# Performance work log

Measured on AMD Instinct MI355X. Metric: run time of the kernel, lower is better.

The kernel has to match this reference:

```python
import jax, jax.numpy as jnp
import numpy as np

TEMPERATURE = 0.5  # init temperature; attn_drop=0.0 so dropout is identity


def setup_inputs() -> dict:
    key = jax.random.key(0)
    k1, k2, k3 = jax.random.split(key, 3)
    B, H, N, D = 4, 8, 2048, 64
    q = jax.random.normal(k1, (B, H, N, D), dtype=jnp.float32)
    k = jax.random.normal(k2, (B, H, N, D), dtype=jnp.float32)
    v = jax.random.normal(k3, (B, H, N, D), dtype=jnp.float32)
    scale = jnp.asarray(D ** -0.5, dtype=jnp.float32)
    return {"q": q, "k": k, "v": v, "scale": scale}


def reference(q, k, v, scale):
    # logits: [B,H,N,N]
    logits = jnp.einsum("bhqd,bhkd->bhqk", q, k) * scale
    # first softmax acts as a soft mask over keys
    soft_mask = jax.nn.softmax(logits / TEMPERATURE, axis=-1)
    # second softmax over masked logits (elementwise product, NOT matmul)
    attn = jax.nn.softmax(logits * soft_mask, axis=-1)
    # dropout with p=0.0 is identity
    out = jnp.einsum("bhqk,bhkd->bhqd", attn, v)
    return out
```

## Files before the change

### kernel.cpp

```cpp
#include <hip/hip_runtime.h>


typedef _Float16 f16;
typedef f16 f16x8 __attribute__((ext_vector_type(8)));
typedef f16 f16x4 __attribute__((ext_vector_type(4)));
typedef float f32x4 __attribute__((ext_vector_type(4)));

#define MFMA32(a, b, c) __builtin_amdgcn_mfma_f32_16x16x32_f16((a), (b), (c), 0, 0, 0)
#define MFMA16(a, b, c) __builtin_amdgcn_mfma_f32_16x16x16f16((a), (b), (c), 0, 0, 0)
#define EXP2(x) __builtin_amdgcn_exp2f(x)

#define N_CTX 2048
#define DH 64
#define KT 64
#define NKT_G 16
#define ROWS 128
#define QS 72
#define KSB (KT * QS)
#define SMEM_BYTES (4 * 2 * KSB * 2 + 2048)

#define C2 2.885390081777927f

__device__ inline unsigned pk(float a, float b) {
    typedef __fp16 fp16x2_t __attribute__((ext_vector_type(2)));
    union { fp16x2_t v; unsigned u; } x;
    x.v = __builtin_amdgcn_cvt_pkrtz(a, b);
    return x.u;
}

__global__ __launch_bounds__(256)
void stk_prep(const float* __restrict__ kg, const float* __restrict__ vg,
              f16* __restrict__ wsK, f16* __restrict__ wsV) {
    const int bid = blockIdx.x, tid = threadIdx.x;
    if (bid < 2048) {
        int g = bid * 256 + tid;
        int bh = g >> 14, key = (g >> 3) & 2047, c = g & 7;
        const float* src = kg + (((size_t)bh * 2048 + key) << 6) + c * 8;
        float4 a = *(const float4*)src;
        float4 b = *(const float4*)(src + 4);
        uint4 o;
        o.x = pk(a.x, a.y); o.y = pk(a.z, a.w);
        o.z = pk(b.x, b.y); o.w = pk(b.z, b.w);
        *(uint4*)&wsK[(((size_t)bh * 2048 + key) << 6) + c * 8] = o;
    } else {
        __shared__ f16 lds[DH * QS];
        const int bid2 = bid - 2048;
        const int bh = bid2 >> 5, t = bid2 & 31;
        const int p = tid >> 3, dseg = tid & 7, d0 = dseg * 8;
        const int c0 = ((p >> 1) & 3) * 16 + ((p >> 3) & 3) * 4 + (p & 1) * 2;
        const float* base = vg + (((size_t)(bh * 2048 + t * 64 + 2 * p)) << 6) + d0;
        float4 a0 = *(const float4*)(base);
        float4 a1 = *(const float4*)(base + 4);
        float4 b0 = *(const float4*)(base + 64);
        float4 b1 = *(const float4*)(base + 68);
        #pragma unroll
        for (int j = 0; j < 4; ++j) {
            *(unsigned*)&lds[(d0 + j) * QS + c0] =
                pk(((const float*)&a0)[j], ((const float*)&b0)[j]);
            *(unsigned*)&lds[(d0 + 4 + j) * QS + c0] =
                pk(((const float*)&a1)[j], ((const float*)&b1)[j]);
        }
        __syncthreads();
        const int d = tid >> 2, cs = tid & 3;
        f16x8 r0 = *(const f16x8*)&lds[d * QS + cs * 16];
        f16x8 r1 = *(const f16x8*)&lds[d * QS + cs * 16 + 8];
        f16* dst = wsV + ((((size_t)bh * 32 + t) << 6) + d) * 64 + cs * 16;
        *(f16x8*)(dst) = r0;
        *(f16x8*)(dst + 8) = r1;
    }
}

__global__ __launch_bounds__(1024, 8)
void stk_attn_mfma(const float* __restrict__ qg, const f16* __restrict__ wsK,
                   const f16* __restrict__ wsV, const float* __restrict__ sg,
                   float* __restrict__ og) {
    extern __shared__ f16 smem[];

    const int tid  = threadIdx.x;
    const int wv   = tid >> 6;
    const int grp  = wv >> 3;
    const int wv7  = wv & 7;
    const int lane = tid & 63;
    const int l15  = lane & 15;
    const int q4   = lane >> 4;
    const int tg   = (wv7 << 6) | lane;
    const int bh   = blockIdx.x & 31;
    const int q0   = (blockIdx.x >> 5) * ROWS;
    const float scale2 = sg[0] * C2;

    const float* qb = qg + (size_t)bh * N_CTX * DH;
    float*       ob = og + (size_t)bh * N_CTX * DH;
    const f16* wsKh = wsK + ((size_t)bh << 17);
    const f16* wsVh = wsV + ((size_t)bh << 17);
    const int T0 = grp * NKT_G;

    f16x8 aq[2];
    {
        const float* qrow = qb + (size_t)(q0 + wv7 * 16 + l15) * DH;
        #pragma unroll
        for (int kc = 0; kc < 2; ++kc) {
            float4 a0 = *(const float4*)&qrow[kc * 32 + q4 * 8];
            float4 a1 = *(const float4*)&qrow[kc * 32 + q4 * 8 + 4];
            union { f16x8 h; unsigned u[4]; } A;
            A.u[0] = pk(a0.x * scale2, a0.y * scale2);
            A.u[1] = pk(a0.z * scale2, a0.w * scale2);
            A.u[2] = pk(a1.x * scale2, a1.y * scale2);
            A.u[3] = pk(a1.z * scale2, a1.w * scale2);
            aq[kc] = A.h;
        }
    }

    f16* const ksBase = smem + grp * (2 * KSB);
    f16* const vtBase = smem + 2 * (2 * KSB) + grp * (2 * KSB);
    float* const sred = (float*)(smem + 4 * (2 * KSB));
    float* const obuf = (float*)smem;

    const int sofs = tg * 8;
    const int wofs = (tg >> 3) * QS + (tg & 7) * 8;

    const f16* const ks_r = ksBase + l15 * QS + q4 * 8;
    const f16* const ksrB = vtBase + l15 * QS + q4 * 8;
    const f16* const vt_r = vtBase + l15 * QS + q4 * 16;

    float s1 = 0.f;
    f16x8 kr2[2];
    kr2[0] = *(const f16x8*)&wsKh[(size_t)T0 * 4096 + sofs];
    kr2[1] = *(const f16x8*)&wsKh[(size_t)(T0 + 1) * 4096 + sofs];
    *(f16x8*)&ksBase[wofs] = kr2[0];
    *(f16x8*)&ksBase[KSB + wofs] = kr2[1];
    kr2[0] = *(const f16x8*)&wsKh[(size_t)(T0 + 2) * 4096 + sofs];
    kr2[1] = *(const f16x8*)&wsKh[(size_t)(T0 + 3) * 4096 + sofs];
    __syncthreads();

    for (int st = 0; st < 8; ++st) {
        f16* const nxtb = (st & 1) ? ksBase : vtBase;
        const f16* const crd = (st & 1) ? ksrB : ks_r;
        *(f16x8*)&nxtb[wofs] = kr2[0];
        *(f16x8*)&nxtb[KSB + wofs] = kr2[1];
        {
            int tn = (st + 2 < 8) ? st + 2 : 7;
            kr2[0] = *(const f16x8*)&wsKh[(size_t)(T0 + 2 * tn) * 4096 + sofs];
            kr2[1] = *(const f16x8*)&wsKh[(size_t)(T0 + 2 * tn + 1) * 4096 + sofs];
        }
        __builtin_amdgcn_s_setprio(1);
        #pragma unroll
        for (int kgi = 0; kgi < 8; ++kgi) {
            f16x8 b0 = *(const f16x8*)&crd[kgi * 16 * QS];
            f16x8 b1 = *(const f16x8*)&crd[kgi * 16 * QS + 32];
            f32x4 acc = {0.f, 0.f, 0.f, 0.f};
            acc = MFMA32(b0, aq[0], acc);
            acc = MFMA32(b1, aq[1], acc);
            s1 += (EXP2(acc[0]) + EXP2(acc[1])) + (EXP2(acc[2]) + EXP2(acc[3]));
        }
        __builtin_amdgcn_s_setprio(0);
        __syncthreads();
    }
    s1 += __shfl_xor(s1, 16, 64);
    s1 += __shfl_xor(s1, 32, 64);
    if (lane < 16) sred[(grp << 7) + (wv7 << 4) + lane] = s1;
    __syncthreads();
    s1 += sred[((grp ^ 1) << 7) + (wv7 << 4) + l15];
    const float inv1 = 0.5f / s1;

    f32x4 O[4];
    #pragma unroll
    for (int dt = 0; dt < 4; ++dt) O[dt] = (f32x4){0.f, 0.f, 0.f, 0.f};
    f32x4 Oe = {0.f, 0.f, 0.f, 0.f};
    const f16x4 ones = {(f16)1.f, (f16)1.f, (f16)1.f, (f16)1.f};

    f16* const ks_w = ksBase;
    f16* const vt_w = vtBase;
    f16x8 krh, vrh;
    krh = *(const f16x8*)&wsKh[(size_t)T0 * 4096 + sofs];
    vrh = *(const f16x8*)&wsVh[(size_t)T0 * 4096 + sofs];
    __syncthreads();
    *(f16x8*)&ks_w[wofs] = krh;
    *(f16x8*)&vt_w[wofs] = vrh;
    krh = *(const f16x8*)&wsKh[(size_t)(T0 + 1) * 4096 + sofs];
    vrh = *(const f16x8*)&wsVh[(size_t)(T0 + 1) * 4096 + sofs];
    __syncthreads();

    for (int kt = 0; kt < NKT_G; ++kt) {
        const int cur = (kt & 1) * KSB, nxt = KSB - cur;
        *(f16x8*)&ks_w[nxt + wofs] = krh;
        *(f16x8*)&vt_w[nxt + wofs] = vrh;
        { int tn = (kt + 2 < NKT_G) ? kt + 2 : NKT_G - 1;
          krh = *(const f16x8*)&wsKh[(size_t)(T0 + tn) * 4096 + sofs];
          vrh = *(const f16x8*)&wsVh[(size_t)(T0 + tn) * 4096 + sofs]; }
        __builtin_amdgcn_s_setprio(1);
        #pragma unroll
        for (int p = 0; p < 2; ++p) {
            f16x4 pfr[2];
            #pragma unroll
            for (int h = 0; h < 2; ++h) {
                const int kgi = p * 2 + h;
                f16x8 b0 = *(const f16x8*)&ks_r[cur + kgi * 16 * QS];
                f16x8 b1 = *(const f16x8*)&ks_r[cur + kgi * 16 * QS + 32];
                f32x4 acc = {0.f, 0.f, 0.f, 0.f};
                acc = MFMA32(b0, aq[0], acc);
                acc = MFMA32(b1, aq[1], acc);
                float e2r[4];
                #pragma unroll
                for (int r = 0; r < 4; ++r) {
                    float a  = acc[r];
                    float e1 = EXP2(a);
                    e2r[r] = EXP2((a * e1) * inv1);
                }
                union { f16x4 hh; unsigned u[2]; } P;
                P.u[0] = pk(e2r[0], e2r[1]);
                P.u[1] = pk(e2r[2], e2r[3]);
                pfr[h] = P.hh;
                Oe = MFMA16(ones, pfr[h], Oe);
            }
            #pragma unroll
            for (int dt = 0; dt < 4; ++dt) {
                f16x8 av = *(const f16x8*)&vt_r[cur + dt * 16 * QS + p * 8];
                f16x4 alo = __builtin_shufflevector(av, av, 0, 1, 2, 3);
                f16x4 ahi = __builtin_shufflevector(av, av, 4, 5, 6, 7);
                O[dt] = MFMA16(alo, pfr[0], O[dt]);
                O[dt] = MFMA16(ahi, pfr[1], O[dt]);
            }
        }
        __builtin_amdgcn_s_setprio(0);
        __syncthreads();
    }

    const int rec = tg * 20;
    if (grp) {
        #pragma unroll
        for (int dt = 0; dt < 4; ++dt)
            *(f32x4*)&obuf[rec + dt * 4] = O[dt];
        obuf[rec + 16] = Oe[0];
    }
    __syncthreads();
    if (!grp) {
        #pragma unroll
        for (int dt = 0; dt < 4; ++dt)
            O[dt] += *(const f32x4*)&obuf[rec + dt * 4];
        const float invl2 = 1.0f / (Oe[0] + obuf[rec + 16]);
        const size_t orow = (size_t)(q0 + wv7 * 16 + l15) * DH;
        #pragma unroll
        for (int dt = 0; dt < 4; ++dt) {
            float4 o;
            o.x = O[dt][0] * invl2;
            o.y = O[dt][1] * invl2;
            o.z = O[dt][2] * invl2;
            o.w = O[dt][3] * invl2;
            *(float4*)&ob[orow + dt * 16 + q4 * 4] = o;
        }
    }
}

extern "C" void kernel_launch(void* const* d_in, const int* in_sizes, int n_in,
                              void* d_out, int out_size, void* d_ws, size_t ws_size,
                              hipStream_t stream) {
    const float* q = (const float*)d_in[0];
    const float* k = (const float*)d_in[1];
    const float* v = (const float*)d_in[2];
    const float* s = (const float*)d_in[3];
    float* out = (float*)d_out;
    f16* wsK = (f16*)d_ws;
    f16* wsV = wsK + (size_t)32 * N_CTX * DH;
    stk_prep<<<dim3(3072), dim3(256), 0, stream>>>(k, v, wsK, wsV);
    dim3 grid(32 * 16);
    stk_attn_mfma<<<grid, 1024, SMEM_BYTES, stream>>>(q, wsK, wsV, s, out);
}
```

Before: 170.3 us.

## Fuse K fp32-to-fp16 conversion into attention kernel, drop K prep pass

Measured after the change: 206.6 us. 1.21x slower.

```diff
diff --git a/kernel.cpp b/kernel.cpp
--- a/kernel.cpp
+++ b/kernel.cpp
@@ -29,49 +29,35 @@
 }
 
 __global__ __launch_bounds__(256)
-void stk_prep(const float* __restrict__ kg, const float* __restrict__ vg,
-              f16* __restrict__ wsK, f16* __restrict__ wsV) {
-    const int bid = blockIdx.x, tid = threadIdx.x;
-    if (bid < 2048) {
-        int g = bid * 256 + tid;
-        int bh = g >> 14, key = (g >> 3) & 2047, c = g & 7;
-        const float* src = kg + (((size_t)bh * 2048 + key) << 6) + c * 8;
-        float4 a = *(const float4*)src;
-        float4 b = *(const float4*)(src + 4);
-        uint4 o;
-        o.x = pk(a.x, a.y); o.y = pk(a.z, a.w);
-        o.z = pk(b.x, b.y); o.w = pk(b.z, b.w);
-        *(uint4*)&wsK[(((size_t)bh * 2048 + key) << 6) + c * 8] = o;
-    } else {
-        __shared__ f16 lds[DH * QS];
-        const int bid2 = bid - 2048;
-        const int bh = bid2 >> 5, t = bid2 & 31;
-        const int p = tid >> 3, dseg = tid & 7, d0 = dseg * 8;
-        const int c0 = ((p >> 1) & 3) * 16 + ((p >> 3) & 3) * 4 + (p & 1) * 2;
-        const float* base = vg + (((size_t)(bh * 2048 + t * 64 + 2 * p)) << 6) + d0;
-        float4 a0 = *(const float4*)(base);
-        float4 a1 = *(const float4*)(base + 4);
-        float4 b0 = *(const float4*)(base + 64);
-        float4 b1 = *(const float4*)(base + 68);
-        #pragma unroll
-        for (int j = 0; j < 4; ++j) {
-            *(unsigned*)&lds[(d0 + j) * QS + c0] =
-                pk(((const float*)&a0)[j], ((const float*)&b0)[j]);
-            *(unsigned*)&lds[(d0 + 4 + j) * QS + c0] =
-                pk(((const float*)&a1)[j], ((const float*)&b1)[j]);
-        }
-        __syncthreads();
-        const int d = tid >> 2, cs = tid & 3;
-        f16x8 r0 = *(const f16x8*)&lds[d * QS + cs * 16];
-        f16x8 r1 = *(const f16x8*)&lds[d * QS + cs * 16 + 8];
-        f16* dst = wsV + ((((size_t)bh * 32 + t) << 6) + d) * 64 + cs * 16;
-        *(f16x8*)(dst) = r0;
-        *(f16x8*)(dst + 8) = r1;
-    }
+void stk_prep(const float* __restrict__ vg, f16* __restrict__ wsV) {
+    __shared__ f16 lds[DH * QS];
+    const int tid = threadIdx.x;
+    const int bh = blockIdx.x >> 5, t = blockIdx.x & 31;
+    const int p = tid >> 3, dseg = tid & 7, d0 = dseg * 8;
+    const int c0 = ((p >> 1) & 3) * 16 + ((p >> 3) & 3) * 4 + (p & 1) * 2;
+    const float* base = vg + (((size_t)(bh * 2048 + t * 64 + 2 * p)) << 6) + d0;
+    float4 a0 = *(const float4*)(base);
+    float4 a1 = *(const float4*)(base + 4);
+    float4 b0 = *(const float4*)(base + 64);
+    float4 b1 = *(const float4*)(base + 68);
+    #pragma unroll
+    for (int j = 0; j < 4; ++j) {
+        *(unsigned*)&lds[(d0 + j) * QS + c0] =
+            pk(((const float*)&a0)[j], ((const float*)&b0)[j]);
+        *(unsigned*)&lds[(d0 + 4 + j) * QS + c0] =
+            pk(((const float*)&a1)[j], ((const float*)&b1)[j]);
+    }
+    __syncthreads();
+    const int d = tid >> 2, cs = tid & 3;
+    f16x8 r0 = *(const f16x8*)&lds[d * QS + cs * 16];
+    f16x8 r1 = *(const f16x8*)&lds[d * QS + cs * 16 + 8];
+    f16* dst = wsV + ((((size_t)bh * 32 + t) << 6) + d) * 64 + cs * 16;
+    *(f16x8*)(dst) = r0;
+    *(f16x8*)(dst + 8) = r1;
 }
 
 __global__ __launch_bounds__(1024, 8)
-void stk_attn_mfma(const float* __restrict__ qg, const f16* __restrict__ wsK,
+void stk_attn_mfma(const float* __restrict__ qg, const float* __restrict__ kg,
                    const f16* __restrict__ wsV, const float* __restrict__ sg,
                    float* __restrict__ og) {
     extern __shared__ f16 smem[];
@@ -90,7 +76,7 @@
 
     const float* qb = qg + (size_t)bh * N_CTX * DH;
     float*       ob = og + (size_t)bh * N_CTX * DH;
-    const f16* wsKh = wsK + ((size_t)bh << 17);
+    const float* kbg = kg + ((size_t)bh * N_CTX + grp * (NKT_G * KT)) * DH;
     const f16* wsVh = wsV + ((size_t)bh << 17);
     const int T0 = grp * NKT_G;
 
@@ -115,6 +101,13 @@
     float* const sred = (float*)(smem + 4 * (2 * KSB));
     float* const obuf = (float*)smem;
 
+    int kofs[2], gofs[2];
+    #pragma unroll
+    for (int it = 0; it < 2; ++it) {
+        int idx = it * 512 + tg;
+        gofs[it] = (idx >> 4) * DH + (idx & 15) * 4;
+        kofs[it] = (idx >> 4) * QS + (idx & 15) * 4;
+    }
     const int sofs = tg * 8;
     const int wofs = (tg >> 3) * QS + (tg & 7) * 8;
 
@@ -123,24 +116,43 @@
     const f16* const vt_r = vtBase + l15 * QS + q4 * 16;
 
     float s1 = 0.f;
-    f16x8 kr2[2];
-    kr2[0] = *(const f16x8*)&wsKh[(size_t)T0 * 4096 + sofs];
-    kr2[1] = *(const f16x8*)&wsKh[(size_t)(T0 + 1) * 4096 + sofs];
-    *(f16x8*)&ksBase[wofs] = kr2[0];
-    *(f16x8*)&ksBase[KSB + wofs] = kr2[1];
-    kr2[0] = *(const f16x8*)&wsKh[(size_t)(T0 + 2) * 4096 + sofs];
-    kr2[1] = *(const f16x8*)&wsKh[(size_t)(T0 + 3) * 4096 + sofs];
+    float4 kra[2], krb[2];
+    #pragma unroll
+    for (int it = 0; it < 2; ++it) {
+        kra[it] = *(const float4*)&kbg[gofs[it]];
+        krb[it] = *(const float4*)&kbg[KT * DH + gofs[it]];
+    }
+    #pragma unroll
+    for (int it = 0; it < 2; ++it) {
+        *(uint2*)&ksBase[kofs[it]] =
+            make_uint2(pk(kra[it].x, kra[it].y), pk(kra[it].z, kra[it].w));
+        *(uint2*)&ksBase[KSB + kofs[it]] =
+            make_uint2(pk(krb[it].x, krb[it].y), pk(krb[it].z, krb[it].w));
+    }
+    #pragma unroll
+    for (int it = 0; it < 2; ++it) {
+        kra[it] = *(const float4*)&kbg[2 * KT * DH + gofs[it]];
+        krb[it] = *(const float4*)&kbg[3 * KT * DH + gofs[it]];
+    }
     __syncthreads();
 
     for (int st = 0; st < 8; ++st) {
         f16* const nxtb = (st & 1) ? ksBase : vtBase;
         const f16* const crd = (st & 1) ? ksrB : ks_r;
-        *(f16x8*)&nxtb[wofs] = kr2[0];
-        *(f16x8*)&nxtb[KSB + wofs] = kr2[1];
+        #pragma unroll
+        for (int it = 0; it < 2; ++it) {
+            *(uint2*)&nxtb[kofs[it]] =
+                make_uint2(pk(kra[it].x, kra[it].y), pk(kra[it].z, kra[it].w));
+            *(uint2*)&nxtb[KSB + kofs[it]] =
+                make_uint2(pk(krb[it].x, krb[it].y), pk(krb[it].z, krb[it].w));
+        }
         {
             int tn = (st + 2 < 8) ? st + 2 : 7;
-            kr2[0] = *(const f16x8*)&wsKh[(size_t)(T0 + 2 * tn) * 4096 + sofs];
-            kr2[1] = *(const f16x8*)&wsKh[(size_t)(T0 + 2 * tn + 1) * 4096 + sofs];
+            #pragma unroll
+            for (int it = 0; it < 2; ++it) {
+                kra[it] = *(const float4*)&kbg[(size_t)(2 * tn) * KT * DH + gofs[it]];
+                krb[it] = *(const float4*)&kbg[(size_t)(2 * tn + 1) * KT * DH + gofs[it]];
+            }
         }
         __builtin_amdgcn_s_setprio(1);
         #pragma unroll
@@ -170,22 +182,33 @@
 
     f16* const ks_w = ksBase;
     f16* const vt_w = vtBase;
-    f16x8 krh, vrh;
-    krh = *(const f16x8*)&wsKh[(size_t)T0 * 4096 + sofs];
+    f16x8 vrh;
+    #pragma unroll
+    for (int it = 0; it < 2; ++it)
+        kra[it] = *(const float4*)&kbg[gofs[it]];
     vrh = *(const f16x8*)&wsVh[(size_t)T0 * 4096 + sofs];
-    __syncthreads();
-    *(f16x8*)&ks_w[wofs] = krh;
+    #pragma unroll
+    for (int it = 0; it < 2; ++it)
+        *(uint2*)&ks_w[kofs[it]] =
+            make_uint2(pk(kra[it].x, kra[it].y), pk(kra[it].z, kra[it].w));
     *(f16x8*)&vt_w[wofs] = vrh;
-    krh = *(const f16x8*)&wsKh[(size_t)(T0 + 1) * 4096 + sofs];
+    #pragma unroll
+    for (int it = 0; it < 2; ++it)
+        kra[it] = *(const float4*)&kbg[KT * DH + gofs[it]];
     vrh = *(const f16x8*)&wsVh[(size_t)(T0 + 1) * 4096 + sofs];
     __syncthreads();
 
     for (int kt = 0; kt < NKT_G; ++kt) {
         const int cur = (kt & 1) * KSB, nxt = KSB - cur;
-        *(f16x8*)&ks_w[nxt + wofs] = krh;
+        #pragma unroll
+        for (int it = 0; it < 2; ++it)
+            *(uint2*)&ks_w[nxt + kofs[it]] =
+                make_uint2(pk(kra[it].x, kra[it].y), pk(kra[it].z, kra[it].w));
         *(f16x8*)&vt_w[nxt + wofs] = vrh;
         { int tn = (kt + 2 < NKT_G) ? kt + 2 : NKT_G - 1;
-          krh = *(const f16x8*)&wsKh[(size_t)(T0 + tn) * 4096 + sofs];
+          #pragma unroll
+          for (int it = 0; it < 2; ++it)
+              kra[it] = *(const float4*)&kbg[(size_t)tn * KT * DH + gofs[it]];
           vrh = *(const f16x8*)&wsVh[(size_t)(T0 + tn) * 4096 + sofs]; }
         __builtin_amdgcn_s_setprio(1);
         #pragma unroll
@@ -259,9 +282,8 @@
     const float* v = (const float*)d_in[2];
     const float* s = (const float*)d_in[3];
     float* out = (float*)d_out;
-    f16* wsK = (f16*)d_ws;
-    f16* wsV = wsK + (size_t)32 * N_CTX * DH;
-    stk_prep<<<dim3(3072), dim3(256), 0, stream>>>(k, v, wsK, wsV);
+    f16* wsV = (f16*)d_ws;
+    stk_prep<<<dim3(1024), dim3(256), 0, stream>>>(v, wsV);
     dim3 grid(32 * 16);
-    stk_attn_mfma<<<grid, 1024, SMEM_BYTES, stream>>>(q, wsK, wsV, s, out);
-}
+    stk_attn_mfma<<<grid, 1024, SMEM_BYTES, stream>>>(q, k, wsV, s, out);
+}
```

## Move first-softmax row-sum pass into prep kernel with wider key-split grid

Applied to the files above, without the earlier changes.

After: 544.6 us. 3.2x slower.

```diff
diff --git a/kernel.cpp b/kernel.cpp
--- a/kernel.cpp
+++ b/kernel.cpp
@@ -14,10 +14,11 @@
 #define DH 64
 #define KT 64
 #define NKT_G 16
-#define ROWS 128
 #define QS 72
 #define KSB (KT * QS)
-#define SMEM_BYTES (4 * 2 * KSB * 2 + 2048)
+#define SMEM_A 18432
+#define SMEM_B (4 * 2 * KSB * 2)
+#define WS_HALF ((size_t)32 * N_CTX * DH)
 
 #define C2 2.885390081777927f
 
@@ -28,25 +29,19 @@
     return x.u;
 }
 
-__global__ __launch_bounds__(256)
-void stk_prep(const float* __restrict__ kg, const float* __restrict__ vg,
-              f16* __restrict__ wsK, f16* __restrict__ wsV) {
+__global__ __launch_bounds__(512, 8)
+void stk_p1(const float* __restrict__ qg, const float* __restrict__ kg,
+            const float* __restrict__ vg, const float* __restrict__ sg,
+            f16* __restrict__ wsK, f16* __restrict__ wsV,
+            float* __restrict__ wsS) {
+    extern __shared__ f16 smem[];
     const int bid = blockIdx.x, tid = threadIdx.x;
-    if (bid < 2048) {
-        int g = bid * 256 + tid;
-        int bh = g >> 14, key = (g >> 3) & 2047, c = g & 7;
-        const float* src = kg + (((size_t)bh * 2048 + key) << 6) + c * 8;
-        float4 a = *(const float4*)src;
-        float4 b = *(const float4*)(src + 4);
-        uint4 o;
-        o.x = pk(a.x, a.y); o.y = pk(a.z, a.w);
-        o.z = pk(b.x, b.y); o.w = pk(b.z, b.w);
-        *(uint4*)&wsK[(((size_t)bh * 2048 + key) << 6) + c * 8] = o;
-    } else {
-        __shared__ f16 lds[DH * QS];
-        const int bid2 = bid - 2048;
-        const int bh = bid2 >> 5, t = bid2 & 31;
-        const int p = tid >> 3, dseg = tid & 7, d0 = dseg * 8;
+
+    if (bid < 512) {
+        const int bh = bid >> 4, t = ((bid & 15) << 1) | (tid >> 8);
+        const int t2 = tid & 255;
+        f16* lds = smem + (tid >> 8) * (DH * QS);
+        const int p = t2 >> 3, dseg = t2 & 7, d0 = dseg * 8;
         const int c0 = ((p >> 1) & 3) * 16 + ((p >> 3) & 3) * 4 + (p & 1) * 2;
         const float* base = vg + (((size_t)(bh * 2048 + t * 64 + 2 * p)) << 6) + d0;
         float4 a0 = *(const float4*)(base);
@@ -61,19 +56,105 @@
                 pk(((const float*)&a1)[j], ((const float*)&b1)[j]);
         }
         __syncthreads();
-        const int d = tid >> 2, cs = tid & 3;
+        const int d = t2 >> 2, cs = t2 & 3;
         f16x8 r0 = *(const f16x8*)&lds[d * QS + cs * 16];
         f16x8 r1 = *(const f16x8*)&lds[d * QS + cs * 16 + 8];
         f16* dst = wsV + ((((size_t)bh * 32 + t) << 6) + d) * 64 + cs * 16;
         *(f16x8*)(dst) = r0;
         *(f16x8*)(dst + 8) = r1;
-    }
+        return;
+    }
+
+    const int idx = bid - 512;
+    const int bh = idx & 31, qt = (idx >> 5) & 15, g = idx >> 9;
+    const int wv = tid >> 6, lane = tid & 63, l15 = lane & 15, q4 = lane >> 4;
+    const int q0 = qt * 128;
+    const float scale2 = sg[0] * C2;
+    const float* qb  = qg + (size_t)bh * N_CTX * DH;
+    const float* kbg = kg + ((size_t)bh * N_CTX + g * (NKT_G * KT)) * DH;
+    f16* const wsKg  = wsK + ((size_t)bh << 17) + (size_t)g * (NKT_G * KT) * DH;
+    const bool sw = (qt == 0);
+
+    f16x8 aq[2];
+    {
+        const float* qrow = qb + (size_t)(q0 + wv * 16 + l15) * DH;
+        #pragma unroll
+        for (int kc = 0; kc < 2; ++kc) {
+            float4 a0 = *(const float4*)&qrow[kc * 32 + q4 * 8];
+            float4 a1 = *(const float4*)&qrow[kc * 32 + q4 * 8 + 4];
+            union { f16x8 h; unsigned u[4]; } A;
+            A.u[0] = pk(a0.x * scale2, a0.y * scale2);
+            A.u[1] = pk(a0.z * scale2, a0.w * scale2);
+            A.u[2] = pk(a1.x * scale2, a1.y * scale2);
+            A.u[3] = pk(a1.z * scale2, a1.w * scale2);
+            aq[kc] = A.h;
+        }
+    }
+
+    int kofs[2], gofs[2];
+    #pragma unroll
+    for (int it = 0; it < 2; ++it) {
+        int i2 = it * 512 + tid;
+        gofs[it] = (i2 >> 4) * DH + (i2 & 15) * 4;
+        kofs[it] = (i2 >> 4) * QS + (i2 & 15) * 4;
+    }
+    f16* const ksBase = smem;
+    const f16* const ks_r = ksBase + l15 * QS + q4 * 8;
+
+    float s1 = 0.f;
+    float4 kr[2];
+    #pragma unroll
+    for (int it = 0; it < 2; ++it)
+        kr[it] = *(const float4*)&kbg[gofs[it]];
+    #pragma unroll
+    for (int it = 0; it < 2; ++it) {
+        uint2 c = make_uint2(pk(kr[it].x, kr[it].y), pk(kr[it].z, kr[it].w));
+        *(uint2*)&ksBase[kofs[it]] = c;
+        if (sw) *(uint2*)&wsKg[gofs[it]] = c;
+    }
+    #pragma unroll
+    for (int it = 0; it < 2; ++it)
+        kr[it] = *(const float4*)&kbg[KT * DH + gofs[it]];
+    __syncthreads();
+
+    for (int kt = 0; kt < NKT_G; ++kt) {
+        const int cur = (kt & 1) * KSB, nxt = KSB - cur;
+        const int tw = (kt + 1 < NKT_G) ? kt + 1 : NKT_G - 1;
+        #pragma unroll
+        for (int it = 0; it < 2; ++it) {
+            uint2 c = make_uint2(pk(kr[it].x, kr[it].y), pk(kr[it].z, kr[it].w));
+            *(uint2*)&ksBase[nxt + kofs[it]] = c;
+            if (sw) *(uint2*)&wsKg[(size_t)tw * (KT * DH) + gofs[it]] = c;
+        }
+        {
+            int tn = (kt + 2 < NKT_G) ? kt + 2 : NKT_G - 1;
+            #pragma unroll
+            for (int it = 0; it < 2; ++it)
+                kr[it] = *(const float4*)&kbg[(size_t)tn * KT * DH + gofs[it]];
+        }
+        __builtin_amdgcn_s_setprio(1);
+        #pragma unroll
+        for (int kgi = 0; kgi < 4; ++kgi) {
+            f16x8 b0 = *(const f16x8*)&ks_r[cur + kgi * 16 * QS];
+            f16x8 b1 = *(const f16x8*)&ks_r[cur + kgi * 16 * QS + 32];
+            f32x4 acc = {0.f, 0.f, 0.f, 0.f};
+            acc = MFMA32(b0, aq[0], acc);
+            acc = MFMA32(b1, aq[1], acc);
+            s1 += (EXP2(acc[0]) + EXP2(acc[1])) + (EXP2(acc[2]) + EXP2(acc[3]));
+        }
+        __builtin_amdgcn_s_setprio(0);
+        __syncthreads();
+    }
+    s1 += __shfl_xor(s1, 16, 64);
+    s1 += __shfl_xor(s1, 32, 64);
+    if (lane < 16)
+        wsS[(size_t)g * 65536 + (size_t)bh * 2048 + q0 + wv * 16 + lane] = s1;
 }
 
 __global__ __launch_bounds__(1024, 8)
-void stk_attn_mfma(const float* __restrict__ qg, const f16* __restrict__ wsK,
-                   const f16* __restrict__ wsV, const float* __restrict__ sg,
-                   float* __restrict__ og) {
+void stk_p2(const float* __restrict__ qg, const f16* __restrict__ wsK,
+            const f16* __restrict__ wsV, const float* __restrict__ wsS,
+            const float* __restrict__ sg, float* __restrict__ og) {
     extern __shared__ f16 smem[];
 
     const int tid  = threadIdx.x;
@@ -85,7 +166,7 @@
     const int q4   = lane >> 4;
     const int tg   = (wv7 << 6) | lane;
     const int bh   = blockIdx.x & 31;
-    const int q0   = (blockIdx.x >> 5) * ROWS;
+    const int q0   = (blockIdx.x >> 5) * 128;
     const float scale2 = sg[0] * C2;
 
     const float* qb = qg + (size_t)bh * N_CTX * DH;
@@ -112,54 +193,15 @@
 
     f16* const ksBase = smem + grp * (2 * KSB);
     f16* const vtBase = smem + 2 * (2 * KSB) + grp * (2 * KSB);
-    float* const sred = (float*)(smem + 4 * (2 * KSB));
     float* const obuf = (float*)smem;
 
     const int sofs = tg * 8;
     const int wofs = (tg >> 3) * QS + (tg & 7) * 8;
-
     const f16* const ks_r = ksBase + l15 * QS + q4 * 8;
-    const f16* const ksrB = vtBase + l15 * QS + q4 * 8;
     const f16* const vt_r = vtBase + l15 * QS + q4 * 16;
 
-    float s1 = 0.f;
-    f16x8 kr2[2];
-    kr2[0] = *(const f16x8*)&wsKh[(size_t)T0 * 4096 + sofs];
-    kr2[1] = *(const f16x8*)&wsKh[(size_t)(T0 + 1) * 4096 + sofs];
-    *(f16x8*)&ksBase[wofs] = kr2[0];
-    *(f16x8*)&ksBase[KSB + wofs] = kr2[1];
-    kr2[0] = *(const f16x8*)&wsKh[(size_t)(T0 + 2) * 4096 + sofs];
-    kr2[1] = *(const f16x8*)&wsKh[(size_t)(T0 + 3) * 4096 + sofs];
-    __syncthreads();
-
-    for (int st = 0; st < 8; ++st) {
-        f16* const nxtb = (st & 1) ? ksBase : vtBase;
-        const f16* const crd = (st & 1) ? ksrB : ks_r;
-        *(f16x8*)&nxtb[wofs] = kr2[0];
-        *(f16x8*)&nxtb[KSB + wofs] = kr2[1];
-        {
-            int tn = (st + 2 < 8) ? st + 2 : 7;
-            kr2[0] = *(const f16x8*)&wsKh[(size_t)(T0 + 2 * tn) * 4096 + sofs];
-            kr2[1] = *(const f16x8*)&wsKh[(size_t)(T0 + 2 * tn + 1) * 4096 + sofs];
-        }
-        __builtin_amdgcn_s_setprio(1);
-        #pragma unroll
-        for (int kgi = 0; kgi < 8; ++kgi) {
-            f16x8 b0 = *(const f16x8*)&crd[kgi * 16 * QS];
-            f16x8 b1 = *(const f16x8*)&crd[kgi * 16 * QS + 32];
-            f32x4 acc = {0.f, 0.f, 0.f, 0.f};
-            acc = MFMA32(b0, aq[0], acc);
-            acc = MFMA32(b1, aq[1], acc);
-            s1 += (EXP2(acc[0]) + EXP2(acc[1])) + (EXP2(acc[2]) + EXP2(acc[3]));
-        }
-        __builtin_amdgcn_s_setprio(0);
-        __syncthreads();
-    }
-    s1 += __shfl_xor(s1, 16, 64);
-    s1 += __shfl_xor(s1, 32, 64);
-    if (lane < 16) sred[(grp << 7) + (wv7 << 4) + lane] = s1;
-    __syncthreads();
-    s1 += sred[((grp ^ 1) << 7) + (wv7 << 4) + l15];
+    const size_t srow = (size_t)bh * 2048 + q0 + wv7 * 16 + l15;
+    const float s1 = wsS[srow] + wsS[65536 + srow];
     const float inv1 = 0.5f / s1;
 
     f32x4 O[4];
@@ -173,7 +215,6 @@
     f16x8 krh, vrh;
     krh = *(const f16x8*)&wsKh[(size_t)T0 * 4096 + sofs];
     vrh = *(const f16x8*)&wsVh[(size_t)T0 * 4096 + sofs];
-    __syncthreads();
     *(f16x8*)&ks_w[wofs] = krh;
     *(f16x8*)&vt_w[wofs] = vrh;
     krh = *(const f16x8*)&wsKh[(size_t)(T0 + 1) * 4096 + sofs];
@@ -260,8 +301,8 @@
     const float* s = (const float*)d_in[3];
     float* out = (float*)d_out;
     f16* wsK = (f16*)d_ws;
-    f16* wsV = wsK + (size_t)32 * N_CTX * DH;
-    stk_prep<<<dim3(3072), dim3(256), 0, stream>>>(k, v, wsK, wsV);
-    dim3 grid(32 * 16);
-    stk_attn_mfma<<<grid, 1024, SMEM_BYTES, stream>>>(q, wsK, wsV, s, out);
+    f16* wsV = wsK + WS_HALF;
+    float* wsS = (float*)(wsV + WS_HALF);
+    stk_p1<<<dim3(1536), dim3(512), SMEM_A, stream>>>(q, k, v, s, wsK, wsV, wsS);
+    stk_p2<<<dim3(512), dim3(1024), SMEM_B, stream>>>(q, wsK, wsV, wsS, s, out);
 }
```
